# Kernel optimization log

Measured on AMD Instinct MI355X. Metric: run time of the kernel, lower is better.

Reference implementation:

```python
import jax, jax.numpy as jnp
import numpy as np

DIM = 1024
D_STATE = 16
D_CONV = 4
EXPAND = 2
D_INNER = EXPAND * DIM          # 2048
DT_RANK = DIM // 16             # 64 (mamba default: ceil(d_model/16))
BATCH = 2
SEQ = 2048


def setup_inputs() -> dict:
    key = jax.random.key(0)
    ks = jax.random.split(key, 32)
    s = 0.02
    def mk(k, shape):
        return jax.random.normal(k, shape, jnp.float32) * s
    inp = {}
    inp["hidden_state"] = jax.random.normal(ks[0], (BATCH, SEQ, DIM), jnp.float32)
    inp["mask"] = jax.random.bernoulli(ks[1], 0.7, (BATCH, SEQ)).astype(jnp.float32)
    inp["mask_proj_w"] = mk(ks[2], (DIM, 1))
    inp["mask_proj_b"] = mk(ks[3], (DIM,))
    i = 4
    A_init = jnp.log(jnp.broadcast_to(jnp.arange(1, D_STATE + 1, dtype=jnp.float32), (D_INNER, D_STATE)))
    for p in ("f", "b"):
        inp[p + "_in_w"]   = mk(ks[i], (2 * D_INNER, DIM)); i += 1
        inp[p + "_conv_w"] = mk(ks[i], (D_INNER, D_CONV)); i += 1
        inp[p + "_conv_b"] = mk(ks[i], (D_INNER,)); i += 1
        inp[p + "_xproj_w"] = mk(ks[i], (DT_RANK + 2 * D_STATE, D_INNER)); i += 1
        inp[p + "_dt_w"]   = mk(ks[i], (D_INNER, DT_RANK)); i += 1
        inp[p + "_dt_b"]   = mk(ks[i], (D_INNER,)) + 1.0  # softplus(~1) -> moderate dt
        i += 1
        inp[p + "_A_log"]  = A_init
        inp[p + "_D"]      = jnp.ones((D_INNER,), jnp.float32)
        inp[p + "_out_w"]  = mk(ks[i], (DIM, D_INNER)); i += 1
    return inp


def _mamba(x, in_w, conv_w, conv_b, xproj_w, dt_w, dt_b, A_log, Dp, out_w):
    # x: [B, L, DIM]
    Bsz = x.shape[0]
    xz = x @ in_w.T                                  # [B, L, 2*D_INNER]
    xi, z = jnp.split(xz, 2, axis=-1)
    # causal depthwise conv1d over time
    xc = jnp.transpose(xi, (0, 2, 1))                # [B, D_INNER, L]
    xc = jax.lax.conv_general_dilated(
        xc, conv_w[:, None, :], window_strides=(1,),
        padding=[(D_CONV - 1, 0)], feature_group_count=D_INNER)
    xc = xc + conv_b[None, :, None]
    u = jax.nn.silu(jnp.transpose(xc, (0, 2, 1)))    # [B, L, D_INNER]
    dbc = u @ xproj_w.T                              # [B, L, DT_RANK + 2*D_STATE]
    dt, Bm, Cm = jnp.split(dbc, [DT_RANK, DT_RANK + D_STATE], axis=-1)
    delta = jax.nn.softplus(dt @ dt_w.T + dt_b)      # [B, L, D_INNER]
    A = -jnp.exp(A_log)                              # [D_INNER, D_STATE]
    dA = jnp.exp(jnp.einsum('bld,dn->bldn', delta, A))
    dBu = jnp.einsum('bld,bln,bld->bldn', delta, Bm, u)
    def step(h, inps):
        dA_t, dBu_t, C_t = inps                      # [B,D_INNER,D_STATE], [B,D_INNER,D_STATE], [B,D_STATE]
        h = dA_t * h + dBu_t
        y = jnp.einsum('bdn,bn->bd', h, C_t)
        return h, y
    h0 = jnp.zeros((Bsz, D_INNER, D_STATE), x.dtype)
    xs = (jnp.moveaxis(dA, 1, 0), jnp.moveaxis(dBu, 1, 0), jnp.moveaxis(Cm, 1, 0))
    _, ys = jax.lax.scan(step, h0, xs)               # ys: [L, B, D_INNER]
    y = jnp.moveaxis(ys, 0, 1) + u * Dp              # [B, L, D_INNER]
    y = y * jax.nn.silu(z)
    return y @ out_w.T                               # [B, L, DIM]


def reference(hidden_state, mask, mask_proj_w, mask_proj_b,
              f_in_w, f_conv_w, f_conv_b, f_xproj_w, f_dt_w, f_dt_b, f_A_log, f_D, f_out_w,
              b_in_w, b_conv_w, b_conv_b, b_xproj_w, b_dt_w, b_dt_b, b_A_log, b_D, b_out_w):
    m = mask[..., None]                              # [B, L, 1]
    mask_features = m @ mask_proj_w.T + mask_proj_b  # [B, L, DIM]
    x_masked = hidden_state * m + mask_features * (1.0 - m)
    forward_out = _mamba(x_masked, f_in_w, f_conv_w, f_conv_b, f_xproj_w,
                         f_dt_w, f_dt_b, f_A_log, f_D, f_out_w)
    backward_out = jnp.flip(
        _mamba(jnp.flip(x_masked, 1), b_in_w, b_conv_w, b_conv_b, b_xproj_w,
               b_dt_w, b_dt_b, b_A_log, b_D, b_out_w), 1)
    ssm_output = forward_out + backward_out
    return ssm_output * m + hidden_state * (1.0 - m)
```

## Files before the change

### kernel.cpp

```cpp
#include <hip/hip_runtime.h>
#include <hip/hip_bf16.h>
#include <stdint.h>

typedef unsigned short u16;
using bf16x8 = __attribute__((ext_vector_type(8))) short;
using f32x4  = __attribute__((ext_vector_type(4))) float;
typedef unsigned short u16x4 __attribute__((ext_vector_type(4)));

#define AS1 __attribute__((address_space(1)))
#define AS3 __attribute__((address_space(3)))

__device__ __forceinline__ float bf2f(u16 x) {
    union { unsigned int u; float f; } v; v.u = ((unsigned int)x) << 16; return v.f;
}
__device__ __forceinline__ u16 f2bf(float f) {
    union { float f; unsigned int u; } v; v.f = f;
    return (u16)((v.u + 0x7fffu + ((v.u >> 16) & 1u)) >> 16);
}

#define ACT_NONE 0
#define ACT_SOFTPLUS 1

__global__ __launch_bounds__(256) void gemm_bt_kernel(
    const u16* __restrict__ A, int lda,
    const u16* __restrict__ B,
    float* __restrict__ Cf, u16* __restrict__ Cb,
    const float* __restrict__ bias,
    int ldc, int M, int N, int K, int Nreal,
    int flipA, int flipC, int act, int kSlices,
    const float* __restrict__ addC, const float* __restrict__ hid,
    const float* __restrict__ msk)
{
    __shared__ __align__(16) u16 As[2][128 * 64];
    __shared__ __align__(16) u16 Bs[2][128 * 64];

    const int tid  = threadIdx.x;
    const int bm   = blockIdx.y * 128;
    const int bn   = blockIdx.x * 128;
    const int lane = tid & 63;
    const int wid  = tid >> 6;
    const int wr   = (wid >> 1) * 64;
    const int wc   = (wid & 1) * 64;
    const int l15  = lane & 15;
    const int l4   = lane >> 4;

    const int kLen = K / kSlices;
    const int kt0  = (blockIdx.z * kLen) >> 6;
    const int nK   = kLen >> 6;

    f32x4 acc[4][4];
    const f32x4 vzero = {0.f, 0.f, 0.f, 0.f};
    #pragma unroll
    for (int i = 0; i < 4; ++i)
        #pragma unroll
        for (int j = 0; j < 4; ++j) acc[i][j] = vzero;

    auto stage = [&](int buf, int kt) {
        #pragma unroll
        for (int i = 0; i < 4; ++i) {
            int off  = i * 4096 + tid * 16;
            int row  = off >> 7;
            int colB = off & 127;
            int rowG = bm + row;
            if (flipA) { int b = rowG >> 11; int l = rowG & 2047; rowG = (b << 11) + (2047 - l); }
            const char* src = (const char*)A + ((size_t)rowG * lda + ((size_t)kt << 6)) * 2 + colB;
            __builtin_amdgcn_global_load_lds((const AS1 unsigned int*)src,
                                             (AS3 unsigned int*)((char*)As[buf] + off), 16, 0, 0);
        }
        #pragma unroll
        for (int i = 0; i < 4; ++i) {
            int off  = i * 4096 + tid * 16;
            int row  = off >> 7;
            int colB = off & 127;
            int rowG = bn + row;
            const char* src = (const char*)B + ((size_t)rowG * K + ((size_t)kt << 6)) * 2 + colB;
            __builtin_amdgcn_global_load_lds((const AS1 unsigned int*)src,
                                             (AS3 unsigned int*)((char*)Bs[buf] + off), 16, 0, 0);
        }
    };

    stage(0, kt0);
    __syncthreads();

    int cur = 0;
    for (int t = 0; t < nK; ++t) {
        if (t + 1 < nK) stage(cur ^ 1, kt0 + t + 1);

        #pragma unroll
        for (int kk = 0; kk < 2; ++kk) {
            bf16x8 af[4], bfr[4];
            #pragma unroll
            for (int mt = 0; mt < 4; ++mt) {
                int row = wr + mt * 16 + l15;
                af[mt] = *(const bf16x8*)((const char*)As[cur] + row * 128 + kk * 64 + l4 * 16);
            }
            #pragma unroll
            for (int nt = 0; nt < 4; ++nt) {
                int row = wc + nt * 16 + l15;
                bfr[nt] = *(const bf16x8*)((const char*)Bs[cur] + row * 128 + kk * 64 + l4 * 16);
            }
            #pragma unroll
            for (int mt = 0; mt < 4; ++mt)
                #pragma unroll
                for (int nt = 0; nt < 4; ++nt)
                    acc[mt][nt] = __builtin_amdgcn_mfma_f32_16x16x32_bf16(
                        af[mt], bfr[nt], acc[mt][nt], 0, 0, 0);
        }
        __syncthreads();
        cur ^= 1;
    }

    #pragma unroll
    for (int mt = 0; mt < 4; ++mt) {
        #pragma unroll
        for (int nt = 0; nt < 4; ++nt) {
            int col = bn + wc + nt * 16 + l15;
            if (col >= Nreal) continue;
            #pragma unroll
            for (int r = 0; r < 4; ++r) {
                int rowG = bm + wr + mt * 16 + l4 * 4 + r;
                float v = acc[mt][nt][r];
                if (act == ACT_SOFTPLUS) {
                    v += bias[col];
                    v = fmaxf(v, 0.f) + log1pf(__expf(-fabsf(v)));
                }
                int rw = rowG;
                if (flipC) { int b = rw >> 11; int l = rw & 2047; rw = (b << 11) + (2047 - l); }
                size_t ci = (size_t)rw * ldc + col;
                if (kSlices > 1) {
                    atomicAdd(&Cf[ci], v);
                } else if (addC) {
                    float m = msk[rw];
                    float tot = v + addC[ci];
                    Cf[ci] = tot * m + hid[ci] * (1.f - m);
                } else if (Cb) {
                    Cb[ci] = f2bf(v);
                } else {
                    Cf[ci] = v;
                }
            }
        }
    }
}

__global__ void conv_silu_kernel(const u16* __restrict__ xz,
                                 const float* __restrict__ cw,
                                 const float* __restrict__ cb,
                                 u16* __restrict__ u)
{
    int d  = blockIdx.x * 256 + threadIdx.x;
    int r0 = blockIdx.y * 16;
    float w0 = cw[d*4+0], w1 = cw[d*4+1], w2 = cw[d*4+2], w3 = cw[d*4+3];
    float bias = cb[d];
    float x1, x2, x3;
    if (r0 & 2047) {
        x1 = bf2f(xz[(size_t)(r0-1) * 4096 + d]);
        x2 = bf2f(xz[(size_t)(r0-2) * 4096 + d]);
        x3 = bf2f(xz[(size_t)(r0-3) * 4096 + d]);
    } else { x1 = x2 = x3 = 0.f; }
    #pragma unroll
    for (int i = 0; i < 16; ++i) {
        int r = r0 + i;
        float x0 = bf2f(xz[(size_t)r * 4096 + d]);
        float acc = fmaf(w3, x0, fmaf(w2, x1, fmaf(w1, x2, fmaf(w0, x3, bias))));
        float sig = 1.f / (1.f + __expf(-acc));
        u[(size_t)r * 2048 + d] = f2bf(acc * sig);
        x3 = x2; x2 = x1; x1 = x0;
    }
}

#define NCH 32
#define CSZ 64
#define SUB 16
#define LW  264

__global__ __launch_bounds__(256) void scan_part1(
    const u16* __restrict__ delta, const u16* __restrict__ u,
    const float* __restrict__ dbc, const float* __restrict__ A_log,
    float* __restrict__ P, float* __restrict__ S)
{
    __shared__ __align__(16) u16   dl_s[SUB * LW];
    __shared__ __align__(16) u16   ul_s[SUB * LW];
    __shared__ __align__(16) float b_s[SUB * 16];

    const int tid = threadIdx.x;
    const int d0  = blockIdx.x * 256;
    const int c   = blockIdx.y;
    const int b   = blockIdx.z;
    const int d   = d0 + tid;
    const size_t rbase = (size_t)b * 2048 + c * CSZ;

    float a2[16], h[16], p[16];
    #pragma unroll
    for (int q = 0; q < 4; ++q) {
        float4 al = *(const float4*)&A_log[(size_t)d * 16 + q * 4];
        a2[q*4+0] = -__expf(al.x) * 1.4426950408889634f;
        a2[q*4+1] = -__expf(al.y) * 1.4426950408889634f;
        a2[q*4+2] = -__expf(al.z) * 1.4426950408889634f;
        a2[q*4+3] = -__expf(al.w) * 1.4426950408889634f;
    }
    #pragma unroll
    for (int n = 0; n < 16; ++n) { h[n] = 0.f; p[n] = 1.f; }

    const int sr  = tid >> 4;
    const int sc16 = (tid & 15) * 16;

    for (int sch = 0; sch < CSZ / SUB; ++sch) {
        {
            size_t row = rbase + sch * SUB + sr;
            *(bf16x8*)&dl_s[sr * LW + sc16]     = *(const bf16x8*)&delta[row * 2048 + d0 + sc16];
            *(bf16x8*)&dl_s[sr * LW + sc16 + 8] = *(const bf16x8*)&delta[row * 2048 + d0 + sc16 + 8];
            *(bf16x8*)&ul_s[sr * LW + sc16]     = *(const bf16x8*)&u[row * 2048 + d0 + sc16];
            *(bf16x8*)&ul_s[sr * LW + sc16 + 8] = *(const bf16x8*)&u[row * 2048 + d0 + sc16 + 8];
            if (tid < 64) {
                int r2 = tid >> 2, c4 = (tid & 3) * 4;
                size_t g2 = rbase + sch * SUB + r2;
                *(float4*)&b_s[r2 * 16 + c4] = *(const float4*)&dbc[g2 * 96 + 64 + c4];
            }
        }
        __syncthreads();
        for (int s = 0; s < SUB; ++s) {
            float dv  = bf2f(dl_s[s * LW + tid]);
            float uv  = bf2f(ul_s[s * LW + tid]);
            float dvu = dv * uv;
            const float4* Bp = (const float4*)&b_s[s * 16];
            #pragma unroll
            for (int q = 0; q < 4; ++q) {
                float4 Bq = Bp[q];
                #pragma unroll
                for (int j = 0; j < 4; ++j) {
                    int n = q * 4 + j;
                    float dA = exp2f(dv * a2[n]);
                    h[n] = fmaf(dA, h[n], dvu * ((&Bq.x)[j]));
                    p[n] *= dA;
                }
            }
        }
        __syncthreads();
    }

    size_t base = (((size_t)(b * NCH + c)) << 15) + (size_t)d * 16;
    #pragma unroll
    for (int q = 0; q < 4; ++q) {
        float4 pv = { p[q*4+0], p[q*4+1], p[q*4+2], p[q*4+3] };
        float4 sv = { h[q*4+0], h[q*4+1], h[q*4+2], h[q*4+3] };
        *(float4*)&P[base + q * 4] = pv;
        *(float4*)&S[base + q * 4] = sv;
    }
}

__global__ void scan_part2(const float* __restrict__ P, float* __restrict__ S)
{
    int i  = blockIdx.x * 256 + threadIdx.x;
    int b  = i >> 15;
    int dn = i & 32767;
    size_t base = ((size_t)b * NCH) << 15;
    float h = 0.f;
    #pragma unroll 4
    for (int c = 0; c < NCH; ++c) {
        size_t idx = base + ((size_t)c << 15) + dn;
        float p = P[idx];
        float s = S[idx];
        S[idx] = h;
        h = fmaf(p, h, s);
    }
}

__global__ __launch_bounds__(256) void scan_part3(
    const u16* __restrict__ delta, const u16* __restrict__ u,
    const float* __restrict__ dbc, const u16* __restrict__ xz,
    const float* __restrict__ A_log, const float* __restrict__ Dp,
    const float* __restrict__ Hin, u16* __restrict__ y)
{
    __shared__ __align__(16) u16   dl_s[SUB * LW];
    __shared__ __align__(16) u16   ul_s[SUB * LW];
    __shared__ __align__(16) u16   zl_s[SUB * LW];
    __shared__ __align__(16) float bc_s[SUB * 32];

    const int tid = threadIdx.x;
    const int d0  = blockIdx.x * 256;
    const int c   = blockIdx.y;
    const int b   = blockIdx.z;
    const int d   = d0 + tid;
    const size_t rbase = (size_t)b * 2048 + c * CSZ;

    float a2[16], h[16];
    #pragma unroll
    for (int q = 0; q < 4; ++q) {
        float4 al = *(const float4*)&A_log[(size_t)d * 16 + q * 4];
        a2[q*4+0] = -__expf(al.x) * 1.4426950408889634f;
        a2[q*4+1] = -__expf(al.y) * 1.4426950408889634f;
        a2[q*4+2] = -__expf(al.z) * 1.4426950408889634f;
        a2[q*4+3] = -__expf(al.w) * 1.4426950408889634f;
    }
    {
        size_t base = (((size_t)(b * NCH + c)) << 15) + (size_t)d * 16;
        #pragma unroll
        for (int q = 0; q < 4; ++q) {
            float4 hv = *(const float4*)&Hin[base + q * 4];
            h[q*4+0] = hv.x; h[q*4+1] = hv.y; h[q*4+2] = hv.z; h[q*4+3] = hv.w;
        }
    }
    const float Dd = Dp[d];

    const int sr   = tid >> 4;
    const int sc16 = (tid & 15) * 16;

    for (int sch = 0; sch < CSZ / SUB; ++sch) {
        {
            size_t row = rbase + sch * SUB + sr;
            *(bf16x8*)&dl_s[sr * LW + sc16]     = *(const bf16x8*)&delta[row * 2048 + d0 + sc16];
            *(bf16x8*)&dl_s[sr * LW + sc16 + 8] = *(const bf16x8*)&delta[row * 2048 + d0 + sc16 + 8];
            *(bf16x8*)&ul_s[sr * LW + sc16]     = *(const bf16x8*)&u[row * 2048 + d0 + sc16];
            *(bf16x8*)&ul_s[sr * LW + sc16 + 8] = *(const bf16x8*)&u[row * 2048 + d0 + sc16 + 8];
            *(bf16x8*)&zl_s[sr * LW + sc16]     = *(const bf16x8*)&xz[row * 4096 + 2048 + d0 + sc16];
            *(bf16x8*)&zl_s[sr * LW + sc16 + 8] = *(const bf16x8*)&xz[row * 4096 + 2048 + d0 + sc16 + 8];
            if (tid < 128) {
                int r2 = tid >> 3, c4 = (tid & 7) * 4;
                size_t g2 = rbase + sch * SUB + r2;
                *(float4*)&bc_s[r2 * 32 + c4] = *(const float4*)&dbc[g2 * 96 + 64 + c4];
            }
        }
        __syncthreads();
        for (int s = 0; s < SUB; ++s) {
            float dv  = bf2f(dl_s[s * LW + tid]);
            float uv  = bf2f(ul_s[s * LW + tid]);
            float dvu = dv * uv;
            float yv  = 0.f;
            const float4* Bp = (const float4*)&bc_s[s * 32];
            const float4* Cp = (const float4*)&bc_s[s * 32 + 16];
            #pragma unroll
            for (int q = 0; q < 4; ++q) {
                float4 Bq = Bp[q];
                float4 Cq = Cp[q];
                #pragma unroll
                for (int j = 0; j < 4; ++j) {
                    int n = q * 4 + j;
                    float dA = exp2f(dv * a2[n]);
                    h[n] = fmaf(dA, h[n], dvu * ((&Bq.x)[j]));
                    yv   = fmaf(h[n], ((&Cq.x)[j]), yv);
                }
            }
            float zv  = bf2f(zl_s[s * LW + tid]);
            float sig = 1.f / (1.f + __expf(-zv));
            float out = (yv + uv * Dd) * (zv * sig);
            y[(rbase + sch * SUB + s) * 2048 + d] = f2bf(out);
        }
        __syncthreads();
    }
}

__global__ void blend_kernel(const float* __restrict__ hidden, const float* __restrict__ mask,
                             const float* __restrict__ mw, const float* __restrict__ mb,
                             u16* __restrict__ xm)
{
    size_t i = (size_t)blockIdx.x * 256 + threadIdx.x;
    int r = (int)(i >> 10), c = (int)(i & 1023);
    float m = mask[r];
    float v = hidden[i] * m + (m * mw[c] + mb[c]) * (1.f - m);
    xm[i] = f2bf(v);
}

struct CvtArgs { const float* src[8]; u16* dst[8]; };
__global__ void cvt_weights_kernel(CvtArgs a)
{
    size_t i = (size_t)blockIdx.x * 256 + threadIdx.x;
    if (i < 8388608) {
        int s = (int)(i >> 22);
        size_t j = i & 4194303;
        a.dst[s][j] = f2bf(a.src[s][j]);
    } else if (i < 12582912) {
        size_t k = i - 8388608;
        int s = 2 + (int)(k >> 21);
        size_t j = k & 2097151;
        a.dst[s][j] = f2bf(a.src[s][j]);
    } else if (i < 12845056) {
        size_t k = i - 12582912;
        int s = 4 + (int)(k >> 17);
        size_t j = k & 131071;
        a.dst[s][j] = f2bf(a.src[s][j]);
    } else if (i < 13369344) {
        size_t k = i - 12845056;
        int s = 6 + (int)(k >> 18);
        size_t j = k & 262143;
        int r = (int)(j >> 11), c = (int)(j & 2047);
        a.dst[s][j] = (r < 96) ? f2bf(a.src[s][(size_t)r * 2048 + c]) : (u16)0;
    }
}

__global__ void cvt_dt_kernel(const float* __restrict__ dbc, u16* __restrict__ dst) {
    int i = blockIdx.x * 256 + threadIdx.x;
    int r = i >> 6, c = i & 63;
    dst[i] = f2bf(dbc[(size_t)r * 96 + c]);
}

extern "C" void kernel_launch(void* const* d_in, const int* in_sizes, int n_in,
                              void* d_out, int out_size, void* d_ws, size_t ws_size,
                              hipStream_t stream)
{
    (void)in_sizes; (void)n_in; (void)out_size; (void)ws_size;
    const float* hidden = (const float*)d_in[0];
    const float* mask   = (const float*)d_in[1];
    const float* mpw    = (const float*)d_in[2];
    const float* mpb    = (const float*)d_in[3];

    char* ws = (char*)d_ws;
    size_t off = 0;
    auto alloc = [&](size_t bytes) -> char* {
        char* p = ws + off; off += (bytes + 255) & ~(size_t)255; return p;
    };
    u16*   xm    = (u16*)  alloc(4096ull * 1024 * 2);
    u16*   xz    = (u16*)  alloc(4096ull * 4096 * 2);
    u16*   ub    = (u16*)  alloc(4096ull * 2048 * 2);
    float* dbc   = (float*)alloc(4096ull * 96 * 4);
    u16*   dtb   = (u16*)  alloc(4096ull * 64 * 2);
    u16*   delta = (u16*)  alloc(4096ull * 2048 * 2);
    u16*   yb    = (u16*)  alloc(4096ull * 2048 * 2);
    float* fout  = (float*)alloc(4096ull * 1024 * 4);
    float* Pbuf  = (float*)alloc(2ull * NCH * 2048 * 16 * 4);
    float* Sbuf  = (float*)alloc(2ull * NCH * 2048 * 16 * 4);
    u16* w_in[2]  = { (u16*)alloc(4096ull*1024*2), (u16*)alloc(4096ull*1024*2) };
    u16* w_xp[2]  = { (u16*)alloc(128ull*2048*2),  (u16*)alloc(128ull*2048*2)  };
    u16* w_dt[2]  = { (u16*)alloc(2048ull*64*2),   (u16*)alloc(2048ull*64*2)   };
    u16* w_out[2] = { (u16*)alloc(1024ull*2048*2), (u16*)alloc(1024ull*2048*2) };

    {
        CvtArgs ca;
        ca.src[0] = (const float*)d_in[4];  ca.dst[0] = w_in[0];
        ca.src[1] = (const float*)d_in[13]; ca.dst[1] = w_in[1];
        ca.src[2] = (const float*)d_in[12]; ca.dst[2] = w_out[0];
        ca.src[3] = (const float*)d_in[21]; ca.dst[3] = w_out[1];
        ca.src[4] = (const float*)d_in[8];  ca.dst[4] = w_dt[0];
        ca.src[5] = (const float*)d_in[17]; ca.dst[5] = w_dt[1];
        ca.src[6] = (const float*)d_in[7];  ca.dst[6] = w_xp[0];
        ca.src[7] = (const float*)d_in[16]; ca.dst[7] = w_xp[1];
        cvt_weights_kernel<<<(13369344 + 255) / 256, 256, 0, stream>>>(ca);
    }
    blend_kernel<<<16384, 256, 0, stream>>>(hidden, mask, mpw, mpb, xm);

    for (int dir = 0; dir < 2; ++dir) {
        int base = 4 + dir * 9;
        const float* conv_w = (const float*)d_in[base+1];
        const float* conv_b = (const float*)d_in[base+2];
        const float* dt_b   = (const float*)d_in[base+5];
        const float* A_log  = (const float*)d_in[base+6];
        const float* Dp     = (const float*)d_in[base+7];
        int flip = dir;

        gemm_bt_kernel<<<dim3(32, 32, 1), 256, 0, stream>>>(
            xm, 1024, w_in[dir], nullptr, xz, nullptr, 4096, 4096, 4096, 1024, 4096,
            flip, 0, ACT_NONE, 1, nullptr, nullptr, nullptr);
        conv_silu_kernel<<<dim3(8, 256), 256, 0, stream>>>(xz, conv_w, conv_b, ub);
        hipMemsetAsync(dbc, 0, 4096ull * 96 * 4, stream);
        gemm_bt_kernel<<<dim3(1, 32, 4), 256, 0, stream>>>(
            ub, 2048, w_xp[dir], dbc, nullptr, nullptr, 96, 4096, 128, 2048, 96,
            0, 0, ACT_NONE, 4, nullptr, nullptr, nullptr);
        cvt_dt_kernel<<<(4096*64)/256, 256, 0, stream>>>(dbc, dtb);
        gemm_bt_kernel<<<dim3(16, 32, 1), 256, 0, stream>>>(
            dtb, 64, w_dt[dir], nullptr, delta, dt_b, 2048, 4096, 2048, 64, 2048,
            0, 0, ACT_SOFTPLUS, 1, nullptr, nullptr, nullptr);
        scan_part1<<<dim3(8, NCH, 2), 256, 0, stream>>>(delta, ub, dbc, A_log, Pbuf, Sbuf);
        scan_part2<<<256, 256, 0, stream>>>(Pbuf, Sbuf);
        scan_part3<<<dim3(8, NCH, 2), 256, 0, stream>>>(delta, ub, dbc, xz, A_log, Dp, Sbuf, yb);
        if (dir == 0) {
            gemm_bt_kernel<<<dim3(8, 32, 1), 256, 0, stream>>>(
                yb, 2048, w_out[0], fout, nullptr, nullptr, 1024, 4096, 1024, 2048, 1024,
                0, 0, ACT_NONE, 1, nullptr, nullptr, nullptr);
        } else {
            gemm_bt_kernel<<<dim3(8, 32, 1), 256, 0, stream>>>(
                yb, 2048, w_out[1], (float*)d_out, nullptr, nullptr, 1024, 4096, 1024, 2048, 1024,
                0, 1, ACT_NONE, 1, fout, hidden, mask);
        }
    }
}
```

Measured before the change: 816.2 us.

## Merge both directions' in/out projections into single GEMMs and scan reversed in-place

Instead of flipping the input for the backward Mamba pass, the in-projection weights of both directions are concatenated into one 8192-wide GEMM on the unflipped input. The conv and scan kernels gain a REV template that walks time in reverse. The two directions' y outputs are written side by side, and a single K=4096 out-projection GEMM with concatenated weights computes the sum and applies the mask blend. This removes the separate fout buffer, the flip index math and two GEMM launches. The GEMM also drops LDS double-buffering in favour of a single buffer with a sync before compute, which reduces LDS use per block but loses overlap of global loads with MFMA work.

```diff
diff --git a/kernel.cpp b/kernel.cpp
--- a/kernel.cpp
+++ b/kernel.cpp
@@ -27,12 +27,11 @@
     float* __restrict__ Cf, u16* __restrict__ Cb,
     const float* __restrict__ bias,
     int ldc, int M, int N, int K, int Nreal,
-    int flipA, int flipC, int act, int kSlices,
-    const float* __restrict__ addC, const float* __restrict__ hid,
-    const float* __restrict__ msk)
-{
-    __shared__ __align__(16) u16 As[2][128 * 64];
-    __shared__ __align__(16) u16 Bs[2][128 * 64];
+    int act, int kSlices,
+    const float* __restrict__ hid, const float* __restrict__ msk)
+{
+    __shared__ __align__(16) u16 As[128 * 64];
+    __shared__ __align__(16) u16 Bs[128 * 64];
 
     const int tid  = threadIdx.x;
     const int bm   = blockIdx.y * 128;
@@ -55,36 +54,27 @@
         #pragma unroll
         for (int j = 0; j < 4; ++j) acc[i][j] = vzero;
 
-    auto stage = [&](int buf, int kt) {
+    for (int t = 0; t < nK; ++t) {
+        int kt = kt0 + t;
         #pragma unroll
         for (int i = 0; i < 4; ++i) {
             int off  = i * 4096 + tid * 16;
             int row  = off >> 7;
             int colB = off & 127;
-            int rowG = bm + row;
-            if (flipA) { int b = rowG >> 11; int l = rowG & 2047; rowG = (b << 11) + (2047 - l); }
-            const char* src = (const char*)A + ((size_t)rowG * lda + ((size_t)kt << 6)) * 2 + colB;
+            const char* src = (const char*)A + ((size_t)(bm + row) * lda + ((size_t)kt << 6)) * 2 + colB;
             __builtin_amdgcn_global_load_lds((const AS1 unsigned int*)src,
-                                             (AS3 unsigned int*)((char*)As[buf] + off), 16, 0, 0);
+                                             (AS3 unsigned int*)((char*)As + off), 16, 0, 0);
         }
         #pragma unroll
         for (int i = 0; i < 4; ++i) {
             int off  = i * 4096 + tid * 16;
             int row  = off >> 7;
             int colB = off & 127;
-            int rowG = bn + row;
-            const char* src = (const char*)B + ((size_t)rowG * K + ((size_t)kt << 6)) * 2 + colB;
+            const char* src = (const char*)B + ((size_t)(bn + row) * K + ((size_t)kt << 6)) * 2 + colB;
             __builtin_amdgcn_global_load_lds((const AS1 unsigned int*)src,
-                                             (AS3 unsigned int*)((char*)Bs[buf] + off), 16, 0, 0);
-        }
-    };
-
-    stage(0, kt0);
-    __syncthreads();
-
-    int cur = 0;
-    for (int t = 0; t < nK; ++t) {
-        if (t + 1 < nK) stage(cur ^ 1, kt0 + t + 1);
+                                             (AS3 unsigned int*)((char*)Bs + off), 16, 0, 0);
+        }
+        __syncthreads();
 
         #pragma unroll
         for (int kk = 0; kk < 2; ++kk) {
@@ -92,12 +82,12 @@
             #pragma unroll
             for (int mt = 0; mt < 4; ++mt) {
                 int row = wr + mt * 16 + l15;
-                af[mt] = *(const bf16x8*)((const char*)As[cur] + row * 128 + kk * 64 + l4 * 16);
+                af[mt] = *(const bf16x8*)((const char*)As + row * 128 + kk * 64 + l4 * 16);
             }
             #pragma unroll
             for (int nt = 0; nt < 4; ++nt) {
                 int row = wc + nt * 16 + l15;
-                bfr[nt] = *(const bf16x8*)((const char*)Bs[cur] + row * 128 + kk * 64 + l4 * 16);
+                bfr[nt] = *(const bf16x8*)((const char*)Bs + row * 128 + kk * 64 + l4 * 16);
             }
             #pragma unroll
             for (int mt = 0; mt < 4; ++mt)
@@ -107,7 +97,6 @@
                         af[mt], bfr[nt], acc[mt][nt], 0, 0, 0);
         }
         __syncthreads();
-        cur ^= 1;
     }
 
     #pragma unroll
@@ -118,21 +107,18 @@
             if (col >= Nreal) continue;
             #pragma unroll
             for (int r = 0; r < 4; ++r) {
-                int rowG = bm + wr + mt * 16 + l4 * 4 + r;
+                int rw = bm + wr + mt * 16 + l4 * 4 + r;
                 float v = acc[mt][nt][r];
                 if (act == ACT_SOFTPLUS) {
                     v += bias[col];
                     v = fmaxf(v, 0.f) + log1pf(__expf(-fabsf(v)));
                 }
-                int rw = rowG;
-                if (flipC) { int b = rw >> 11; int l = rw & 2047; rw = (b << 11) + (2047 - l); }
                 size_t ci = (size_t)rw * ldc + col;
                 if (kSlices > 1) {
                     atomicAdd(&Cf[ci], v);
-                } else if (addC) {
+                } else if (hid) {
                     float m = msk[rw];
-                    float tot = v + addC[ci];
-                    Cf[ci] = tot * m + hid[ci] * (1.f - m);
+                    Cf[ci] = v * m + hid[ci] * (1.f - m);
                 } else if (Cb) {
                     Cb[ci] = f2bf(v);
                 } else {
@@ -143,7 +129,8 @@
     }
 }
 
-__global__ void conv_silu_kernel(const u16* __restrict__ xz,
+template<int REV>
+__global__ void conv_silu_kernel(const u16* __restrict__ x,
                                  const float* __restrict__ cw,
                                  const float* __restrict__ cb,
                                  u16* __restrict__ u)
@@ -152,20 +139,37 @@
     int r0 = blockIdx.y * 16;
     float w0 = cw[d*4+0], w1 = cw[d*4+1], w2 = cw[d*4+2], w3 = cw[d*4+3];
     float bias = cb[d];
-    float x1, x2, x3;
-    if (r0 & 2047) {
-        x1 = bf2f(xz[(size_t)(r0-1) * 4096 + d]);
-        x2 = bf2f(xz[(size_t)(r0-2) * 4096 + d]);
-        x3 = bf2f(xz[(size_t)(r0-3) * 4096 + d]);
-    } else { x1 = x2 = x3 = 0.f; }
-    #pragma unroll
-    for (int i = 0; i < 16; ++i) {
-        int r = r0 + i;
-        float x0 = bf2f(xz[(size_t)r * 4096 + d]);
-        float acc = fmaf(w3, x0, fmaf(w2, x1, fmaf(w1, x2, fmaf(w0, x3, bias))));
-        float sig = 1.f / (1.f + __expf(-acc));
-        u[(size_t)r * 2048 + d] = f2bf(acc * sig);
-        x3 = x2; x2 = x1; x1 = x0;
+    if (!REV) {
+        float x1, x2, x3;
+        if (r0 & 2047) {
+            x1 = bf2f(x[(size_t)(r0-1) * 8192 + d]);
+            x2 = bf2f(x[(size_t)(r0-2) * 8192 + d]);
+            x3 = bf2f(x[(size_t)(r0-3) * 8192 + d]);
+        } else { x1 = x2 = x3 = 0.f; }
+        #pragma unroll
+        for (int i = 0; i < 16; ++i) {
+            int r = r0 + i;
+            float x0 = bf2f(x[(size_t)r * 8192 + d]);
+            float acc = fmaf(w3, x0, fmaf(w2, x1, fmaf(w1, x2, fmaf(w0, x3, bias))));
+            float sig = 1.f / (1.f + __expf(-acc));
+            u[(size_t)r * 2048 + d] = f2bf(acc * sig);
+            x3 = x2; x2 = x1; x1 = x0;
+        }
+    } else {
+        int le = (r0 + 15) & 2047;
+        float x1, x2, x3;
+        x1 = (le + 1 < 2048) ? bf2f(x[(size_t)(r0+16) * 8192 + d]) : 0.f;
+        x2 = (le + 2 < 2048) ? bf2f(x[(size_t)(r0+17) * 8192 + d]) : 0.f;
+        x3 = (le + 3 < 2048) ? bf2f(x[(size_t)(r0+18) * 8192 + d]) : 0.f;
+        #pragma unroll
+        for (int i = 15; i >= 0; --i) {
+            int r = r0 + i;
+            float x0 = bf2f(x[(size_t)r * 8192 + d]);
+            float acc = fmaf(w3, x0, fmaf(w2, x1, fmaf(w1, x2, fmaf(w0, x3, bias))));
+            float sig = 1.f / (1.f + __expf(-acc));
+            u[(size_t)r * 2048 + d] = f2bf(acc * sig);
+            x3 = x2; x2 = x1; x1 = x0;
+        }
     }
 }
 
@@ -174,6 +178,7 @@
 #define SUB 16
 #define LW  264
 
+template<int REV>
 __global__ __launch_bounds__(256) void scan_part1(
     const u16* __restrict__ delta, const u16* __restrict__ u,
     const float* __restrict__ dbc, const float* __restrict__ A_log,
@@ -206,24 +211,26 @@
     const int sc16 = (tid & 15) * 16;
 
     for (int sch = 0; sch < CSZ / SUB; ++sch) {
+        const int sch_ = REV ? (CSZ / SUB - 1 - sch) : sch;
         {
-            size_t row = rbase + sch * SUB + sr;
+            size_t row = rbase + sch_ * SUB + sr;
             *(bf16x8*)&dl_s[sr * LW + sc16]     = *(const bf16x8*)&delta[row * 2048 + d0 + sc16];
             *(bf16x8*)&dl_s[sr * LW + sc16 + 8] = *(const bf16x8*)&delta[row * 2048 + d0 + sc16 + 8];
             *(bf16x8*)&ul_s[sr * LW + sc16]     = *(const bf16x8*)&u[row * 2048 + d0 + sc16];
             *(bf16x8*)&ul_s[sr * LW + sc16 + 8] = *(const bf16x8*)&u[row * 2048 + d0 + sc16 + 8];
             if (tid < 64) {
                 int r2 = tid >> 2, c4 = (tid & 3) * 4;
-                size_t g2 = rbase + sch * SUB + r2;
+                size_t g2 = rbase + sch_ * SUB + r2;
                 *(float4*)&b_s[r2 * 16 + c4] = *(const float4*)&dbc[g2 * 96 + 64 + c4];
             }
         }
         __syncthreads();
         for (int s = 0; s < SUB; ++s) {
-            float dv  = bf2f(dl_s[s * LW + tid]);
-            float uv  = bf2f(ul_s[s * LW + tid]);
+            const int s_ = REV ? (SUB - 1 - s) : s;
+            float dv  = bf2f(dl_s[s_ * LW + tid]);
+            float uv  = bf2f(ul_s[s_ * LW + tid]);
             float dvu = dv * uv;
-            const float4* Bp = (const float4*)&b_s[s * 16];
+            const float4* Bp = (const float4*)&b_s[s_ * 16];
             #pragma unroll
             for (int q = 0; q < 4; ++q) {
                 float4 Bq = Bp[q];
@@ -249,6 +256,7 @@
     }
 }
 
+template<int REV>
 __global__ void scan_part2(const float* __restrict__ P, float* __restrict__ S)
 {
     int i  = blockIdx.x * 256 + threadIdx.x;
@@ -257,7 +265,8 @@
     size_t base = ((size_t)b * NCH) << 15;
     float h = 0.f;
     #pragma unroll 4
-    for (int c = 0; c < NCH; ++c) {
+    for (int cc = 0; cc < NCH; ++cc) {
+        int c = REV ? (NCH - 1 - cc) : cc;
         size_t idx = base + ((size_t)c << 15) + dn;
         float p = P[idx];
         float s = S[idx];
@@ -266,9 +275,10 @@
     }
 }
 
+template<int REV>
 __global__ __launch_bounds__(256) void scan_part3(
     const u16* __restrict__ delta, const u16* __restrict__ u,
-    const float* __restrict__ dbc, const u16* __restrict__ xz,
+    const float* __restrict__ dbc, const u16* __restrict__ z,
     const float* __restrict__ A_log, const float* __restrict__ Dp,
     const float* __restrict__ Hin, u16* __restrict__ y)
 {
@@ -307,28 +317,30 @@
     const int sc16 = (tid & 15) * 16;
 
     for (int sch = 0; sch < CSZ / SUB; ++sch) {
+        const int sch_ = REV ? (CSZ / SUB - 1 - sch) : sch;
         {
-            size_t row = rbase + sch * SUB + sr;
+            size_t row = rbase + sch_ * SUB + sr;
             *(bf16x8*)&dl_s[sr * LW + sc16]     = *(const bf16x8*)&delta[row * 2048 + d0 + sc16];
             *(bf16x8*)&dl_s[sr * LW + sc16 + 8] = *(const bf16x8*)&delta[row * 2048 + d0 + sc16 + 8];
             *(bf16x8*)&ul_s[sr * LW + sc16]     = *(const bf16x8*)&u[row * 2048 + d0 + sc16];
             *(bf16x8*)&ul_s[sr * LW + sc16 + 8] = *(const bf16x8*)&u[row * 2048 + d0 + sc16 + 8];
-            *(bf16x8*)&zl_s[sr * LW + sc16]     = *(const bf16x8*)&xz[row * 4096 + 2048 + d0 + sc16];
-            *(bf16x8*)&zl_s[sr * LW + sc16 + 8] = *(const bf16x8*)&xz[row * 4096 + 2048 + d0 + sc16 + 8];
+            *(bf16x8*)&zl_s[sr * LW + sc16]     = *(const bf16x8*)&z[row * 8192 + d0 + sc16];
+            *(bf16x8*)&zl_s[sr * LW + sc16 + 8] = *(const bf16x8*)&z[row * 8192 + d0 + sc16 + 8];
             if (tid < 128) {
                 int r2 = tid >> 3, c4 = (tid & 7) * 4;
-                size_t g2 = rbase + sch * SUB + r2;
+                size_t g2 = rbase + sch_ * SUB + r2;
                 *(float4*)&bc_s[r2 * 32 + c4] = *(const float4*)&dbc[g2 * 96 + 64 + c4];
             }
         }
         __syncthreads();
         for (int s = 0; s < SUB; ++s) {
-            float dv  = bf2f(dl_s[s * LW + tid]);
-            float uv  = bf2f(ul_s[s * LW + tid]);
+            const int s_ = REV ? (SUB - 1 - s) : s;
+            float dv  = bf2f(dl_s[s_ * LW + tid]);
+            float uv  = bf2f(ul_s[s_ * LW + tid]);
             float dvu = dv * uv;
             float yv  = 0.f;
-            const float4* Bp = (const float4*)&bc_s[s * 32];
-            const float4* Cp = (const float4*)&bc_s[s * 32 + 16];
+            const float4* Bp = (const float4*)&bc_s[s_ * 32];
+            const float4* Cp = (const float4*)&bc_s[s_ * 32 + 16];
             #pragma unroll
             for (int q = 0; q < 4; ++q) {
                 float4 Bq = Bp[q];
@@ -341,10 +353,10 @@
                     yv   = fmaf(h[n], ((&Cq.x)[j]), yv);
                 }
             }
-            float zv  = bf2f(zl_s[s * LW + tid]);
+            float zv  = bf2f(zl_s[s_ * LW + tid]);
             float sig = 1.f / (1.f + __expf(-zv));
             float out = (yv + uv * Dd) * (zv * sig);
-            y[(rbase + sch * SUB + s) * 2048 + d] = f2bf(out);
+            y[(rbase + sch_ * SUB + s_) * 4096 + d] = f2bf(out);
         }
         __syncthreads();
     }
@@ -368,12 +380,13 @@
     if (i < 8388608) {
         int s = (int)(i >> 22);
         size_t j = i & 4194303;
-        a.dst[s][j] = f2bf(a.src[s][j]);
+        a.dst[0][i] = f2bf(a.src[s][j]);
     } else if (i < 12582912) {
         size_t k = i - 8388608;
-        int s = 2 + (int)(k >> 21);
+        int s = (int)(k >> 21);
         size_t j = k & 2097151;
-        a.dst[s][j] = f2bf(a.src[s][j]);
+        int n = (int)(j >> 11), kk = (int)(j & 2047);
+        a.dst[2][(size_t)n * 4096 + s * 2048 + kk] = f2bf(a.src[2 + s][j]);
     } else if (i < 12845056) {
         size_t k = i - 12582912;
         int s = 4 + (int)(k >> 17);
@@ -409,34 +422,37 @@
     auto alloc = [&](size_t bytes) -> char* {
         char* p = ws + off; off += (bytes + 255) & ~(size_t)255; return p;
     };
-    u16*   xm    = (u16*)  alloc(4096ull * 1024 * 2);
-    u16*   xz    = (u16*)  alloc(4096ull * 4096 * 2);
-    u16*   ub    = (u16*)  alloc(4096ull * 2048 * 2);
-    float* dbc   = (float*)alloc(4096ull * 96 * 4);
-    u16*   dtb   = (u16*)  alloc(4096ull * 64 * 2);
-    u16*   delta = (u16*)  alloc(4096ull * 2048 * 2);
-    u16*   yb    = (u16*)  alloc(4096ull * 2048 * 2);
-    float* fout  = (float*)alloc(4096ull * 1024 * 4);
-    float* Pbuf  = (float*)alloc(2ull * NCH * 2048 * 16 * 4);
-    float* Sbuf  = (float*)alloc(2ull * NCH * 2048 * 16 * 4);
-    u16* w_in[2]  = { (u16*)alloc(4096ull*1024*2), (u16*)alloc(4096ull*1024*2) };
-    u16* w_xp[2]  = { (u16*)alloc(128ull*2048*2),  (u16*)alloc(128ull*2048*2)  };
-    u16* w_dt[2]  = { (u16*)alloc(2048ull*64*2),   (u16*)alloc(2048ull*64*2)   };
-    u16* w_out[2] = { (u16*)alloc(1024ull*2048*2), (u16*)alloc(1024ull*2048*2) };
+    u16*   xm     = (u16*)  alloc(4096ull * 1024 * 2);
+    u16*   xz     = (u16*)  alloc(4096ull * 8192 * 2);
+    u16*   ub     = (u16*)  alloc(4096ull * 2048 * 2);
+    float* dbc    = (float*)alloc(4096ull * 96 * 4);
+    u16*   dtb    = (u16*)  alloc(4096ull * 64 * 2);
+    u16*   delta  = (u16*)  alloc(4096ull * 2048 * 2);
+    u16*   yb     = (u16*)  alloc(4096ull * 4096 * 2);
+    float* Pbuf   = (float*)alloc(2ull * NCH * 2048 * 16 * 4);
+    float* Sbuf   = (float*)alloc(2ull * NCH * 2048 * 16 * 4);
+    u16*   w_in   = (u16*)  alloc(8192ull * 1024 * 2);
+    u16*   w_out  = (u16*)  alloc(1024ull * 4096 * 2);
+    u16*   w_xp[2] = { (u16*)alloc(128ull*2048*2), (u16*)alloc(128ull*2048*2) };
+    u16*   w_dt[2] = { (u16*)alloc(2048ull*64*2),  (u16*)alloc(2048ull*64*2)  };
 
     {
         CvtArgs ca;
-        ca.src[0] = (const float*)d_in[4];  ca.dst[0] = w_in[0];
-        ca.src[1] = (const float*)d_in[13]; ca.dst[1] = w_in[1];
-        ca.src[2] = (const float*)d_in[12]; ca.dst[2] = w_out[0];
-        ca.src[3] = (const float*)d_in[21]; ca.dst[3] = w_out[1];
-        ca.src[4] = (const float*)d_in[8];  ca.dst[4] = w_dt[0];
-        ca.src[5] = (const float*)d_in[17]; ca.dst[5] = w_dt[1];
-        ca.src[6] = (const float*)d_in[7];  ca.dst[6] = w_xp[0];
-        ca.src[7] = (const float*)d_in[16]; ca.dst[7] = w_xp[1];
+        ca.src[0] = (const float*)d_in[4];  ca.src[1] = (const float*)d_in[13];
+        ca.src[2] = (const float*)d_in[12]; ca.src[3] = (const float*)d_in[21];
+        ca.src[4] = (const float*)d_in[8];  ca.src[5] = (const float*)d_in[17];
+        ca.src[6] = (const float*)d_in[7];  ca.src[7] = (const float*)d_in[16];
+        ca.dst[0] = w_in;  ca.dst[1] = nullptr;
+        ca.dst[2] = w_out; ca.dst[3] = nullptr;
+        ca.dst[4] = w_dt[0]; ca.dst[5] = w_dt[1];
+        ca.dst[6] = w_xp[0]; ca.dst[7] = w_xp[1];
         cvt_weights_kernel<<<(13369344 + 255) / 256, 256, 0, stream>>>(ca);
     }
     blend_kernel<<<16384, 256, 0, stream>>>(hidden, mask, mpw, mpb, xm);
+
+    gemm_bt_kernel<<<dim3(64, 32, 1), 256, 0, stream>>>(
+        xm, 1024, w_in, nullptr, xz, nullptr, 8192, 4096, 8192, 1024, 8192,
+        ACT_NONE, 1, nullptr, nullptr);
 
     for (int dir = 0; dir < 2; ++dir) {
         int base = 4 + dir * 9;
@@ -445,31 +461,34 @@
         const float* dt_b   = (const float*)d_in[base+5];
         const float* A_log  = (const float*)d_in[base+6];
         const float* Dp     = (const float*)d_in[base+7];
-        int flip = dir;
-
-        gemm_bt_kernel<<<dim3(32, 32, 1), 256, 0, stream>>>(
-            xm, 1024, w_in[dir], nullptr, xz, nullptr, 4096, 4096, 4096, 1024, 4096,
-            flip, 0, ACT_NONE, 1, nullptr, nullptr, nullptr);
-        conv_silu_kernel<<<dim3(8, 256), 256, 0, stream>>>(xz, conv_w, conv_b, ub);
+        const u16* xi = xz + dir * 4096;
+        const u16* zp = xz + dir * 4096 + 2048;
+
+        if (dir == 0) conv_silu_kernel<0><<<dim3(8, 256), 256, 0, stream>>>(xi, conv_w, conv_b, ub);
+        else          conv_silu_kernel<1><<<dim3(8, 256), 256, 0, stream>>>(xi, conv_w, conv_b, ub);
+
         hipMemsetAsync(dbc, 0, 4096ull * 96 * 4, stream);
         gemm_bt_kernel<<<dim3(1, 32, 4), 256, 0, stream>>>(
             ub, 2048, w_xp[dir], dbc, nullptr, nullptr, 96, 4096, 128, 2048, 96,
-            0, 0, ACT_NONE, 4, nullptr, nullptr, nullptr);
+            ACT_NONE, 4, nullptr, nullptr);
         cvt_dt_kernel<<<(4096*64)/256, 256, 0, stream>>>(dbc, dtb);
         gemm_bt_kernel<<<dim3(16, 32, 1), 256, 0, stream>>>(
             dtb, 64, w_dt[dir], nullptr, delta, dt_b, 2048, 4096, 2048, 64, 2048,
-            0, 0, ACT_SOFTPLUS, 1, nullptr, nullptr, nullptr);
-        scan_part1<<<dim3(8, NCH, 2), 256, 0, stream>>>(delta, ub, dbc, A_log, Pbuf, Sbuf);
-        scan_part2<<<256, 256, 0, stream>>>(Pbuf, Sbuf);
-        scan_part3<<<dim3(8, NCH, 2), 256, 0, stream>>>(delta, ub, dbc, xz, A_log, Dp, Sbuf, yb);
+            ACT_SOFTPLUS, 1, nullptr, nullptr);
+
+        u16* yd = yb + dir * 2048;
         if (dir == 0) {
-            gemm_bt_kernel<<<dim3(8, 32, 1), 256, 0, stream>>>(
-                yb, 2048, w_out[0], fout, nullptr, nullptr, 1024, 4096, 1024, 2048, 1024,
-                0, 0, ACT_NONE, 1, nullptr, nullptr, nullptr);
+            scan_part1<0><<<dim3(8, NCH, 2), 256, 0, stream>>>(delta, ub, dbc, A_log, Pbuf, Sbuf);
+            scan_part2<0><<<256, 256, 0, stream>>>(Pbuf, Sbuf);
+            scan_part3<0><<<dim3(8, NCH, 2), 256, 0, stream>>>(delta, ub, dbc, zp, A_log, Dp, Sbuf, yd);
         } else {
-            gemm_bt_kernel<<<dim3(8, 32, 1), 256, 0, stream>>>(
-                yb, 2048, w_out[1], (float*)d_out, nullptr, nullptr, 1024, 4096, 1024, 2048, 1024,
-                0, 1, ACT_NONE, 1, fout, hidden, mask);
-        }
-    }
-}
+            scan_part1<1><<<dim3(8, NCH, 2), 256, 0, stream>>>(delta, ub, dbc, A_log, Pbuf, Sbuf);
+            scan_part2<1><<<256, 256, 0, stream>>>(Pbuf, Sbuf);
+            scan_part3<1><<<dim3(8, NCH, 2), 256, 0, stream>>>(delta, ub, dbc, zp, A_log, Dp, Sbuf, yd);
+        }
+    }
+
+    gemm_bt_kernel<<<dim3(8, 32, 1), 256, 0, stream>>>(
+        yb, 4096, w_out, (float*)d_out, nullptr, nullptr, 1024, 4096, 1024, 4096, 1024,
+        ACT_NONE, 1, hidden, mask);
+}
```

Measured after the change: 763.1 us. 6.5% less time.
